# Performance work log

Measured on AMD Instinct MI355X. Metric: run time of the kernel, lower is better.

## Reference

```python
import jax, jax.numpy as jnp
import numpy as np

B = 8
N = 1024


def _sqrtm_psd(P):
    # symmetric PSD matrix square root via eigendecomposition
    w, V = jnp.linalg.eigh(P)
    return (V * jnp.sqrt(jnp.clip(w, 0.0))) @ V.T


def setup_inputs() -> dict:
    key = jax.random.key(0)
    k1, k2, k3 = jax.random.split(key, 3)
    x = jax.random.normal(k1, (1, B, N, 1), dtype=jnp.float32)
    # PSD covariance with nonnegative entries so abs() is a no-op and sqrtm is real
    A = jax.random.uniform(k2, (N, N), dtype=jnp.float32)
    P_u = (A @ A.T) / N
    Q_k = jax.random.uniform(k3, (N, N), dtype=jnp.float32)
    return {"x": x, "P_u": P_u, "Q_k": Q_k}


def reference(x, P_u, Q_k):
    n = x.shape[2]  # N
    # sigma = x.repeat(1,1,1,N): [1,B,N,N]
    sigma0 = jnp.broadcast_to(x, (1, x.shape[1], n, n))
    # p = sqrtm(N * |P_u|)
    p = _sqrtm_psd(n * jnp.abs(P_u))
    # concat(sigma+p, sigma-p) along last dim -> [1,B,N,2N]
    sigma = jnp.concatenate((sigma0 + p, sigma0 - p), axis=3)
    scale = 1.0 / (2 * n)
    x_bar = jnp.mean(sigma, axis=3)  # [1,B,N]
    # Faithful to original: only sigma[0,0] is used for the deviations,
    # while the mean varies with the batch index i2.
    points = sigma[0, 0]  # [N, 2N]
    c = points[None, :, :] - x_bar[0][:, :, None]  # [B, N, 2N]
    S = jnp.einsum('bni,bmi->bnm', c, c)  # sum of 2N outer products per batch
    P_k = S * scale + (Q_k ** 2) * 0.01
    return P_k, jnp.transpose(sigma, (0, 1, 3, 2))


if __name__ == "__main__":
    out = reference(**setup_inputs())
    print(out[0].shape, out[1].shape)
```

## Files before the change

kernel.cpp:

```cpp
#include <hip/hip_runtime.h>
#include <math.h>

#define NN 1024
#define BB 8
#define NS_ITERS 10
#define EPS_SHIFT 4.0f
#define MB (1u<<20)

typedef __attribute__((ext_vector_type(8))) short short8;
typedef __attribute__((ext_vector_type(4))) float floatx4;

__device__ __forceinline__ ushort f2bf(float f) {
    union { float f; uint32_t u; } v; v.f = f;
    uint32_t u = v.u;
    uint32_t r = (u + 0x7fffu + ((u >> 16) & 1u)) >> 16;
    return (ushort)r;
}
__device__ __forceinline__ float bf2f(ushort h) {
    union { uint32_t u; float f; } v; v.u = ((uint32_t)h) << 16;
    return v.f;
}

__device__ __forceinline__ void gload16(const ushort* g, ushort* s) {
    __builtin_amdgcn_global_load_lds(
        (__attribute__((address_space(1))) unsigned int*)(g),
        (__attribute__((address_space(3))) unsigned int*)(s), 16, 0, 0);
}

__device__ __forceinline__ float block_sum(float v) {
    #pragma unroll
    for (int off = 32; off > 0; off >>= 1) v += __shfl_down(v, off, 64);
    __shared__ float red[4];
    int lane = threadIdx.x & 63, wid = threadIdx.x >> 6;
    if (lane == 0) red[wid] = v;
    __syncthreads();
    float t = 0.f;
    if (threadIdx.x == 0) t = red[0] + red[1] + red[2] + red[3];
    return t;
}

__global__ __launch_bounds__(256) void matvec_abs(const float* __restrict__ pu,
                                                  const float* __restrict__ x,
                                                  float* __restrict__ y,
                                                  int use_ones) {
    int row = blockIdx.x;
    const float4* pr = (const float4*)(pu + (size_t)row * NN);
    float4 p = pr[threadIdx.x];
    float s;
    if (use_ones) {
        s = fabsf(p.x) + fabsf(p.y) + fabsf(p.z) + fabsf(p.w);
    } else {
        float4 xx = ((const float4*)x)[threadIdx.x];
        s = fabsf(p.x) * xx.x + fabsf(p.y) * xx.y + fabsf(p.z) * xx.z + fabsf(p.w) * xx.w;
    }
    s = block_sum(s);
    if (threadIdx.x == 0) y[row] = s;
}

__global__ void norm_vec(const float* __restrict__ y, float* __restrict__ v) {
    float ss = 0.f;
    for (int i = threadIdx.x; i < NN; i += 256) { float t = y[i]; ss += t * t; }
    #pragma unroll
    for (int off = 32; off > 0; off >>= 1) ss += __shfl_down(ss, off, 64);
    __shared__ float red[4];
    __shared__ float s_inv;
    int lane = threadIdx.x & 63, wid = threadIdx.x >> 6;
    if (lane == 0) red[wid] = ss;
    __syncthreads();
    if (threadIdx.x == 0) s_inv = rsqrtf(red[0] + red[1] + red[2] + red[3]);
    __syncthreads();
    float inv = s_inv;
    for (int i = threadIdx.x; i < NN; i += 256) v[i] = y[i] * inv;
}

__global__ void dot_vec(const float* __restrict__ a, const float* __restrict__ b,
                        float* __restrict__ out) {
    float s = 0.f;
    for (int i = threadIdx.x; i < NN; i += 256) s += a[i] * b[i];
    s = block_sum(s);
    if (threadIdx.x == 0) out[0] = s;
}

__global__ __launch_bounds__(256) void deflate_kernel(const float* __restrict__ pu,
                                                      const float* __restrict__ v,
                                                      const float* __restrict__ w,
                                                      float* __restrict__ sc,
                                                      float* __restrict__ D) {
    int idx = blockIdx.x * 256 + threadIdx.x;
    int row = idx >> 8;
    int c0 = (idx & 255) << 2;
    float lam = sc[5];
    float vr = v[row], wr = w[row];
    float4 p = ((const float4*)pu)[idx];
    float4 vc = *(const float4*)(v + c0);
    float4 wc = *(const float4*)(w + c0);
    float4 d;
    d.x = (float)NN * (fabsf(p.x) - vr * wc.x - wr * vc.x + lam * vr * vc.x);
    d.y = (float)NN * (fabsf(p.y) - vr * wc.y - wr * vc.y + lam * vr * vc.y);
    d.z = (float)NN * (fabsf(p.z) - vr * wc.z - wr * vc.z + lam * vr * vc.z);
    d.w = (float)NN * (fabsf(p.w) - vr * wc.w - wr * vc.w + lam * vr * vc.w);
    int dd = row - c0;
    if (dd == 0) d.x += EPS_SHIFT;
    else if (dd == 1) d.y += EPS_SHIFT;
    else if (dd == 2) d.z += EPS_SHIFT;
    else if (dd == 3) d.w += EPS_SHIFT;
    ((float4*)D)[idx] = d;
    float ss = d.x * d.x + d.y * d.y + d.z * d.z + d.w * d.w;
    ss = block_sum(ss);
    if (threadIdx.x == 0) atomicAdd(sc, ss);
}

__global__ void finalize_kernel(float* sc) {
    float c = sqrtf(sc[0]);
    sc[1] = 1.f / c;
    sc[2] = sqrtf(c);
    sc[4] = sqrtf((float)NN * sc[5]);
}

__device__ __forceinline__ void mm_dev(const ushort* __restrict__ Ah,
                                       const ushort* __restrict__ Al,
                                       const ushort* __restrict__ Bh,
                                       const ushort* __restrict__ Bl,
                                       int row0, int col0, int kb, int kc,
                                       float* __restrict__ Cf,
                                       ushort* __restrict__ Chi,
                                       ushort* __restrict__ Clo) {
    __shared__ __align__(16) ushort lds[2 * 4 * 2048];
    const int t = threadIdx.x;
    const int w = t >> 6, l = t & 63;
    const int wr = ((w >> 1) & 1) << 5;
    const int wc = (w & 1) << 5;
    const int fm = l & 15, fq = l >> 4;
    const int srow = l >> 2;
    const int skc = ((l & 3) + srow) & 3;

    const ushort* gsrc = (w == 0) ? Ah : (w == 1) ? Al : (w == 2) ? Bh : Bl;
    const int r0 = (w < 2) ? row0 : col0;
    const ushort* gp = gsrc + (size_t)(r0 + srow) * NN + kb + (skc << 3);

    floatx4 acc[2][2];
    acc[0][0] = (floatx4)0.f; acc[0][1] = (floatx4)0.f;
    acc[1][0] = (floatx4)0.f; acc[1][1] = (floatx4)0.f;

    auto STAGE = [&](int bufi, int koff) {
        ushort* sb = lds + (bufi << 13) + (w << 11);
        #pragma unroll
        for (int rb = 0; rb < 4; ++rb)
            gload16(gp + (size_t)(rb << 4) * NN + koff, sb + (rb << 9));
    };

    const int rot = ((fq - fm) & 3) << 3;
    auto COMPUTE = [&](int bufi) {
        const ushort* Ash = lds + (bufi << 13);
        const ushort* Asl = Ash + 2048;
        const ushort* Bsh = Ash + 4096;
        const ushort* Bsl = Ash + 6144;
        short8 ah0 = *(const short8*)&Ash[((wr + fm) << 5) + rot];
        short8 ah1 = *(const short8*)&Ash[((wr + 16 + fm) << 5) + rot];
        short8 al0 = *(const short8*)&Asl[((wr + fm) << 5) + rot];
        short8 al1 = *(const short8*)&Asl[((wr + 16 + fm) << 5) + rot];
        short8 bh0 = *(const short8*)&Bsh[((wc + fm) << 5) + rot];
        short8 bh1 = *(const short8*)&Bsh[((wc + 16 + fm) << 5) + rot];
        short8 bl0 = *(const short8*)&Bsl[((wc + fm) << 5) + rot];
        short8 bl1 = *(const short8*)&Bsl[((wc + 16 + fm) << 5) + rot];
        acc[0][0] = __builtin_amdgcn_mfma_f32_16x16x32_bf16(ah0, bh0, acc[0][0], 0, 0, 0);
        acc[0][1] = __builtin_amdgcn_mfma_f32_16x16x32_bf16(ah0, bh1, acc[0][1], 0, 0, 0);
        acc[1][0] = __builtin_amdgcn_mfma_f32_16x16x32_bf16(ah1, bh0, acc[1][0], 0, 0, 0);
        acc[1][1] = __builtin_amdgcn_mfma_f32_16x16x32_bf16(ah1, bh1, acc[1][1], 0, 0, 0);
        acc[0][0] = __builtin_amdgcn_mfma_f32_16x16x32_bf16(al0, bh0, acc[0][0], 0, 0, 0);
        acc[0][1] = __builtin_amdgcn_mfma_f32_16x16x32_bf16(al0, bh1, acc[0][1], 0, 0, 0);
        acc[1][0] = __builtin_amdgcn_mfma_f32_16x16x32_bf16(al1, bh0, acc[1][0], 0, 0, 0);
        acc[1][1] = __builtin_amdgcn_mfma_f32_16x16x32_bf16(al1, bh1, acc[1][1], 0, 0, 0);
        acc[0][0] = __builtin_amdgcn_mfma_f32_16x16x32_bf16(ah0, bl0, acc[0][0], 0, 0, 0);
        acc[0][1] = __builtin_amdgcn_mfma_f32_16x16x32_bf16(ah0, bl1, acc[0][1], 0, 0, 0);
        acc[1][0] = __builtin_amdgcn_mfma_f32_16x16x32_bf16(ah1, bl0, acc[1][0], 0, 0, 0);
        acc[1][1] = __builtin_amdgcn_mfma_f32_16x16x32_bf16(ah1, bl1, acc[1][1], 0, 0, 0);
    };

    const int nk = kc >> 5;
    STAGE(0, 0);
    __syncthreads();
    #pragma unroll 1
    for (int kt = 0; kt < nk; kt += 2) {
        STAGE(1, (kt + 1) << 5);
        COMPUTE(0);
        __syncthreads();
        if (kt + 2 < nk) STAGE(0, (kt + 2) << 5);
        COMPUTE(1);
        __syncthreads();
    }

    #pragma unroll
    for (int mi = 0; mi < 2; ++mi) {
        #pragma unroll
        for (int r = 0; r < 4; ++r) {
            int row = row0 + wr + (mi << 4) + (fq << 2) + r;
            #pragma unroll
            for (int ni = 0; ni < 2; ++ni) {
                int col = col0 + wc + (ni << 4) + fm;
                float v = acc[mi][ni][r];
                size_t idx = (size_t)row * NN + col;
                if (Cf) {
                    Cf[idx] = v;
                } else {
                    ushort h = f2bf(v);
                    Chi[idx] = h;
                    Clo[idx] = f2bf(v - bf2f(h));
                }
            }
        }
    }
}

__global__ __launch_bounds__(256) void k_stage1(const ushort* __restrict__ Zh,
                                                const ushort* __restrict__ Zl,
                                                const ushort* __restrict__ Yh,
                                                const ushort* __restrict__ Yl,
                                                float* __restrict__ Mp) {
    int s = blockIdx.z;
    mm_dev(Zh, Zl, Yh, Yl, blockIdx.y * 64, blockIdx.x * 64,
           s * (NN / 2), NN / 2, Mp + (size_t)s * NN * NN, nullptr, nullptr);
}

__global__ __launch_bounds__(256) void k_stage2(const ushort* __restrict__ Yh,
                                                const ushort* __restrict__ Yl,
                                                const ushort* __restrict__ Wh,
                                                const ushort* __restrict__ Wl,
                                                const ushort* __restrict__ Zh,
                                                const ushort* __restrict__ Zl,
                                                ushort* __restrict__ Ynh,
                                                ushort* __restrict__ Ynl,
                                                ushort* __restrict__ Znh,
                                                ushort* __restrict__ Znl) {
    if (blockIdx.z == 0)
        mm_dev(Yh, Yl, Wh, Wl, blockIdx.y * 64, blockIdx.x * 64, 0, NN,
               nullptr, Ynh, Ynl);
    else
        mm_dev(Wh, Wl, Zh, Zl, blockIdx.y * 64, blockIdx.x * 64, 0, NN,
               nullptr, Znh, Znl);
}

__global__ __launch_bounds__(256) void k_final(const ushort* __restrict__ Yh,
                                               const ushort* __restrict__ Yl,
                                               const ushort* __restrict__ Wh,
                                               const ushort* __restrict__ Wl,
                                               float* __restrict__ Yf) {
    mm_dev(Yh, Yl, Wh, Wl, blockIdx.y * 64, blockIdx.x * 64, 0, NN,
           Yf, nullptr, nullptr);
}

__global__ __launch_bounds__(256) void k_wsplit(const float* __restrict__ Mp,
                                                ushort* __restrict__ Wh,
                                                ushort* __restrict__ Wl) {
    int i = blockIdx.x * 256 + threadIdx.x;
    int row = i >> 8, c0 = (i & 255) << 2;
    float4 m0 = ((const float4*)Mp)[i];
    float4 m1 = ((const float4*)Mp)[i + NN * NN / 4];
    float mr[4] = {m0.x + m1.x, m0.y + m1.y, m0.z + m1.z, m0.w + m1.w};
    float wv[4];
    #pragma unroll
    for (int j = 0; j < 4; ++j) {
        float mt = Mp[(size_t)(c0 + j) * NN + row] +
                   Mp[(size_t)(c0 + j) * NN + row + (size_t)NN * NN];
        wv[j] = -0.25f * (mr[j] + mt);
    }
    int dd = row - c0;
    if (dd >= 0 && dd < 4) wv[dd] += 1.5f;
    ushort4 hv, lv;
    ushort* hp = (ushort*)&hv; ushort* lp = (ushort*)&lv;
    #pragma unroll
    for (int j = 0; j < 4; ++j) {
        ushort h = f2bf(wv[j]); hp[j] = h; lp[j] = f2bf(wv[j] - bf2f(h));
    }
    *(ushort4*)&Wh[(size_t)i << 2] = hv;
    *(ushort4*)&Wl[(size_t)i << 2] = lv;
}

__global__ __launch_bounds__(256) void k_wsplit0(const float* __restrict__ D,
                                                 const float* __restrict__ sc,
                                                 ushort* __restrict__ Yh,
                                                 ushort* __restrict__ Yl,
                                                 ushort* __restrict__ Wh,
                                                 ushort* __restrict__ Wl) {
    int i = blockIdx.x * 256 + threadIdx.x;
    int row = i >> 8, c0 = (i & 255) << 2;
    float invc = sc[1];
    float4 d = ((const float4*)D)[i];
    float yv[4] = {d.x * invc, d.y * invc, d.z * invc, d.w * invc};
    ushort4 yh, yl, wh, wl;
    ushort* yhp = (ushort*)&yh; ushort* ylp = (ushort*)&yl;
    ushort* whp = (ushort*)&wh; ushort* wlp = (ushort*)&wl;
    int dd = row - c0;
    #pragma unroll
    for (int j = 0; j < 4; ++j) {
        float y = yv[j];
        ushort h = f2bf(y); yhp[j] = h; ylp[j] = f2bf(y - bf2f(h));
        float wv = ((dd == j) ? 1.5f : 0.f) - 0.5f * y;
        ushort h2 = f2bf(wv); whp[j] = h2; wlp[j] = f2bf(wv - bf2f(h2));
    }
    *(ushort4*)&Yh[(size_t)i << 2] = yh;
    *(ushort4*)&Yl[(size_t)i << 2] = yl;
    *(ushort4*)&Wh[(size_t)i << 2] = wh;
    *(ushort4*)&Wl[(size_t)i << 2] = wl;
}

__global__ __launch_bounds__(256) void out0_kernel(const float* __restrict__ x,
                                                   const float* __restrict__ pu,
                                                   const float* __restrict__ qk,
                                                   float* __restrict__ out) {
    int i = blockIdx.x * blockDim.x + threadIdx.x;
    int rem = i & (NN * NN / 4 - 1);
    int b = i >> 18;
    int n = rem >> 8;
    int m4 = (rem & 255) << 2;
    float dn = x[n] - x[b * NN + n];
    float4 x0v = *(const float4*)(x + m4);
    float4 xbv = *(const float4*)(x + b * NN + m4);
    float4 pv = ((const float4*)pu)[rem];
    float4 qv = ((const float4*)qk)[rem];
    float4 o;
    o.x = dn * (x0v.x - xbv.x) + fabsf(pv.x) + 0.01f * qv.x * qv.x;
    o.y = dn * (x0v.y - xbv.y) + fabsf(pv.y) + 0.01f * qv.y * qv.y;
    o.z = dn * (x0v.z - xbv.z) + fabsf(pv.z) + 0.01f * qv.z * qv.z;
    o.w = dn * (x0v.w - xbv.w) + fabsf(pv.w) + 0.01f * qv.w * qv.w;
    ((float4*)out)[i] = o;
}

__global__ __launch_bounds__(256) void k_out1(const float* __restrict__ x,
                                              const float* __restrict__ Yf,
                                              const float* __restrict__ sc,
                                              const float* __restrict__ v,
                                              float* __restrict__ out1) {
    int i = blockIdx.x * 256 + threadIdx.x;
    int j = i >> 8, i0 = (i & 255) << 2;
    float s = 0.5f * sc[2], s1v = sc[4] * v[j];
    float4 yr = *(const float4*)(Yf + (size_t)j * NN + i0);
    float yc0 = Yf[(size_t)(i0 + 0) * NN + j];
    float yc1 = Yf[(size_t)(i0 + 1) * NN + j];
    float yc2 = Yf[(size_t)(i0 + 2) * NN + j];
    float yc3 = Yf[(size_t)(i0 + 3) * NN + j];
    float4 vc = *(const float4*)(v + i0);
    float4 p;
    p.x = s * (yr.x + yc0) + s1v * vc.x;
    p.y = s * (yr.y + yc1) + s1v * vc.y;
    p.z = s * (yr.z + yc2) + s1v * vc.z;
    p.w = s * (yr.w + yc3) + s1v * vc.w;
    #pragma unroll
    for (int b = 0; b < BB; ++b) {
        float4 xv = *(const float4*)(x + b * NN + i0);
        float4 a, m;
        a.x = xv.x + p.x; a.y = xv.y + p.y; a.z = xv.z + p.z; a.w = xv.w + p.w;
        m.x = xv.x - p.x; m.y = xv.y - p.y; m.z = xv.z - p.z; m.w = xv.w - p.w;
        float* base = out1 + (size_t)b * 2 * NN * NN;
        *(float4*)(base + (size_t)j * NN + i0) = a;
        *(float4*)(base + (size_t)(NN + j) * NN + i0) = m;
    }
}

extern "C" void kernel_launch(void* const* d_in, const int* in_sizes, int n_in,
                              void* d_out, int out_size, void* d_ws, size_t ws_size,
                              hipStream_t stream) {
    const float* x  = (const float*)d_in[0];
    const float* pu = (const float*)d_in[1];
    const float* qk = (const float*)d_in[2];
    float* out = (float*)d_out;
    char* ws = (char*)d_ws;

    float* Mp = (float*)ws;
    float* D  = Mp;
    float* Yf = Mp;
    ushort* hi[5]; ushort* lo[5];
    for (int k = 0; k < 5; ++k) {
        hi[k] = (ushort*)(ws + (size_t)8 * MB + (size_t)k * 4 * MB);
        lo[k] = (ushort*)(ws + (size_t)8 * MB + (size_t)k * 4 * MB + 2 * MB);
    }
    float* vv = (float*)(ws + (size_t)28 * MB);
    float* vw = (float*)(ws + (size_t)28 * MB + 4096);
    float* vt = (float*)(ws + (size_t)28 * MB + 8192);
    float* sc = (float*)(ws + (size_t)28 * MB + 12288);

    hipMemsetAsync(sc, 0, 64, stream);
    matvec_abs<<<NN, 256, 0, stream>>>(pu, vv, vt, 1);
    norm_vec<<<1, 256, 0, stream>>>(vt, vv);
    matvec_abs<<<NN, 256, 0, stream>>>(pu, vv, vt, 0);
    norm_vec<<<1, 256, 0, stream>>>(vt, vv);
    matvec_abs<<<NN, 256, 0, stream>>>(pu, vv, vw, 0);
    dot_vec<<<1, 256, 0, stream>>>(vv, vw, sc + 5);
    deflate_kernel<<<NN * NN / 4 / 256, 256, 0, stream>>>(pu, vv, vw, sc, D);
    finalize_kernel<<<1, 1, 0, stream>>>(sc);

    k_wsplit0<<<NN * NN / 4 / 256, 256, 0, stream>>>(D, sc, hi[0], lo[0], hi[1], lo[1]);
    k_stage2<<<dim3(16, 16, 1), 256, 0, stream>>>(hi[0], lo[0], hi[1], lo[1],
                                                  hi[0], lo[0],
                                                  hi[2], lo[2], hi[3], lo[3]);
    int Y = 2, Z = 1, f0 = 0, f1 = 3, f2 = 4;

    for (int it = 1; it < NS_ITERS; ++it) {
        int W = f0;
        k_stage1<<<dim3(16, 16, 2), 256, 0, stream>>>(hi[Z], lo[Z], hi[Y], lo[Y], Mp);
        k_wsplit<<<NN * NN / 4 / 256, 256, 0, stream>>>(Mp, hi[W], lo[W]);
        if (it + 1 < NS_ITERS) {
            int Yn = f1, Zn = f2;
            k_stage2<<<dim3(16, 16, 2), 256, 0, stream>>>(
                hi[Y], lo[Y], hi[W], lo[W], hi[Z], lo[Z],
                hi[Yn], lo[Yn], hi[Zn], lo[Zn]);
            f0 = Y; f1 = Z; f2 = W;
            Y = Yn; Z = Zn;
        } else {
            k_final<<<dim3(16, 16, 1), 256, 0, stream>>>(hi[Y], lo[Y], hi[W], lo[W], Yf);
        }
    }

    out0_kernel<<<(BB * NN * NN / 4) / 256, 256, 0, stream>>>(x, pu, qk, out);
    k_out1<<<NN * NN / 4 / 256, 256, 0, stream>>>(x, Yf, sc, vv,
                                                  out + (size_t)BB * NN * NN);
}
```

Before: 680.7 us.

## Enlarge GEMM tiles to 128x128 with 4x4 MFMA per wave and tile swizzle

The split-bf16 matmul device function moves from 64x64 block tiles to 128x128 tiles, so each wave computes a 64x64 sub-tile with 4x4 accumulators. This raises arithmetic intensity per LDS load and cuts global traffic. A block-index swizzle is added for L2 locality, and the grids shrink from 16x16 to 8x8. The LDS rotation swizzle is removed, which may bring back bank conflicts. With fewer blocks (64 or 128 on a GPU with many CUs), occupancy and load balance may suffer.

```diff
diff --git a/kernel.cpp b/kernel.cpp
--- a/kernel.cpp
+++ b/kernel.cpp
@@ -125,56 +125,55 @@
                                        float* __restrict__ Cf,
                                        ushort* __restrict__ Chi,
                                        ushort* __restrict__ Clo) {
-    __shared__ __align__(16) ushort lds[2 * 4 * 2048];
+    __shared__ __align__(16) ushort lds[2 * 4 * 4096];
     const int t = threadIdx.x;
     const int w = t >> 6, l = t & 63;
-    const int wr = ((w >> 1) & 1) << 5;
-    const int wc = (w & 1) << 5;
+    const int wr = ((w >> 1) & 1) << 6;
+    const int wc = (w & 1) << 6;
     const int fm = l & 15, fq = l >> 4;
     const int srow = l >> 2;
-    const int skc = ((l & 3) + srow) & 3;
+    const int scol = (l & 3) << 3;
 
     const ushort* gsrc = (w == 0) ? Ah : (w == 1) ? Al : (w == 2) ? Bh : Bl;
     const int r0 = (w < 2) ? row0 : col0;
-    const ushort* gp = gsrc + (size_t)(r0 + srow) * NN + kb + (skc << 3);
-
-    floatx4 acc[2][2];
-    acc[0][0] = (floatx4)0.f; acc[0][1] = (floatx4)0.f;
-    acc[1][0] = (floatx4)0.f; acc[1][1] = (floatx4)0.f;
+    const ushort* gp = gsrc + (size_t)(r0 + srow) * NN + kb + scol;
+
+    floatx4 acc[4][4];
+    #pragma unroll
+    for (int mi = 0; mi < 4; ++mi)
+        #pragma unroll
+        for (int ni = 0; ni < 4; ++ni) acc[mi][ni] = (floatx4)0.f;
 
     auto STAGE = [&](int bufi, int koff) {
-        ushort* sb = lds + (bufi << 13) + (w << 11);
+        ushort* sb = lds + (bufi << 14) + (w << 12);
         #pragma unroll
-        for (int rb = 0; rb < 4; ++rb)
+        for (int rb = 0; rb < 8; ++rb)
             gload16(gp + (size_t)(rb << 4) * NN + koff, sb + (rb << 9));
     };
 
-    const int rot = ((fq - fm) & 3) << 3;
     auto COMPUTE = [&](int bufi) {
-        const ushort* Ash = lds + (bufi << 13);
-        const ushort* Asl = Ash + 2048;
-        const ushort* Bsh = Ash + 4096;
-        const ushort* Bsl = Ash + 6144;
-        short8 ah0 = *(const short8*)&Ash[((wr + fm) << 5) + rot];
-        short8 ah1 = *(const short8*)&Ash[((wr + 16 + fm) << 5) + rot];
-        short8 al0 = *(const short8*)&Asl[((wr + fm) << 5) + rot];
-        short8 al1 = *(const short8*)&Asl[((wr + 16 + fm) << 5) + rot];
-        short8 bh0 = *(const short8*)&Bsh[((wc + fm) << 5) + rot];
-        short8 bh1 = *(const short8*)&Bsh[((wc + 16 + fm) << 5) + rot];
-        short8 bl0 = *(const short8*)&Bsl[((wc + fm) << 5) + rot];
-        short8 bl1 = *(const short8*)&Bsl[((wc + 16 + fm) << 5) + rot];
-        acc[0][0] = __builtin_amdgcn_mfma_f32_16x16x32_bf16(ah0, bh0, acc[0][0], 0, 0, 0);
-        acc[0][1] = __builtin_amdgcn_mfma_f32_16x16x32_bf16(ah0, bh1, acc[0][1], 0, 0, 0);
-        acc[1][0] = __builtin_amdgcn_mfma_f32_16x16x32_bf16(ah1, bh0, acc[1][0], 0, 0, 0);
-        acc[1][1] = __builtin_amdgcn_mfma_f32_16x16x32_bf16(ah1, bh1, acc[1][1], 0, 0, 0);
-        acc[0][0] = __builtin_amdgcn_mfma_f32_16x16x32_bf16(al0, bh0, acc[0][0], 0, 0, 0);
-        acc[0][1] = __builtin_amdgcn_mfma_f32_16x16x32_bf16(al0, bh1, acc[0][1], 0, 0, 0);
-        acc[1][0] = __builtin_amdgcn_mfma_f32_16x16x32_bf16(al1, bh0, acc[1][0], 0, 0, 0);
-        acc[1][1] = __builtin_amdgcn_mfma_f32_16x16x32_bf16(al1, bh1, acc[1][1], 0, 0, 0);
-        acc[0][0] = __builtin_amdgcn_mfma_f32_16x16x32_bf16(ah0, bl0, acc[0][0], 0, 0, 0);
-        acc[0][1] = __builtin_amdgcn_mfma_f32_16x16x32_bf16(ah0, bl1, acc[0][1], 0, 0, 0);
-        acc[1][0] = __builtin_amdgcn_mfma_f32_16x16x32_bf16(ah1, bl0, acc[1][0], 0, 0, 0);
-        acc[1][1] = __builtin_amdgcn_mfma_f32_16x16x32_bf16(ah1, bl1, acc[1][1], 0, 0, 0);
+        const ushort* Ash = lds + (bufi << 14);
+        const ushort* Asl = Ash + 4096;
+        const ushort* Bsh = Ash + 8192;
+        const ushort* Bsl = Ash + 12288;
+        short8 ah[4], al[4], bh[4], bl[4];
+        #pragma unroll
+        for (int i = 0; i < 4; ++i) {
+            const int ra = ((wr + (i << 4) + fm) << 5) + (fq << 3);
+            const int rb = ((wc + (i << 4) + fm) << 5) + (fq << 3);
+            ah[i] = *(const short8*)&Ash[ra];
+            al[i] = *(const short8*)&Asl[ra];
+            bh[i] = *(const short8*)&Bsh[rb];
+            bl[i] = *(const short8*)&Bsl[rb];
+        }
+        #pragma unroll
+        for (int mi = 0; mi < 4; ++mi)
+            #pragma unroll
+            for (int ni = 0; ni < 4; ++ni) {
+                acc[mi][ni] = __builtin_amdgcn_mfma_f32_16x16x32_bf16(ah[mi], bh[ni], acc[mi][ni], 0, 0, 0);
+                acc[mi][ni] = __builtin_amdgcn_mfma_f32_16x16x32_bf16(al[mi], bh[ni], acc[mi][ni], 0, 0, 0);
+                acc[mi][ni] = __builtin_amdgcn_mfma_f32_16x16x32_bf16(ah[mi], bl[ni], acc[mi][ni], 0, 0, 0);
+            }
     };
 
     const int nk = kc >> 5;
@@ -191,12 +190,12 @@
     }
 
     #pragma unroll
-    for (int mi = 0; mi < 2; ++mi) {
+    for (int mi = 0; mi < 4; ++mi) {
         #pragma unroll
         for (int r = 0; r < 4; ++r) {
             int row = row0 + wr + (mi << 4) + (fq << 2) + r;
             #pragma unroll
-            for (int ni = 0; ni < 2; ++ni) {
+            for (int ni = 0; ni < 4; ++ni) {
                 int col = col0 + wc + (ni << 4) + fm;
                 float v = acc[mi][ni][r];
                 size_t idx = (size_t)row * NN + col;
@@ -212,41 +211,51 @@
     }
 }
 
-__global__ __launch_bounds__(256) void k_stage1(const ushort* __restrict__ Zh,
-                                                const ushort* __restrict__ Zl,
-                                                const ushort* __restrict__ Yh,
-                                                const ushort* __restrict__ Yl,
-                                                float* __restrict__ Mp) {
+__device__ __forceinline__ void tile_swizzle(int& row0, int& col0) {
+    int flat = blockIdx.y * 8 + blockIdx.x;
+    int p = flat & 7;
+    int i = flat >> 3;
+    int by = ((p >> 1) << 1) + (i >> 2);
+    int bx = ((p & 1) << 2) + (i & 3);
+    row0 = by << 7;
+    col0 = bx << 7;
+}
+
+__global__ __launch_bounds__(256, 2) void k_stage1(const ushort* __restrict__ Zh,
+                                                   const ushort* __restrict__ Zl,
+                                                   const ushort* __restrict__ Yh,
+                                                   const ushort* __restrict__ Yl,
+                                                   float* __restrict__ Mp) {
     int s = blockIdx.z;
-    mm_dev(Zh, Zl, Yh, Yl, blockIdx.y * 64, blockIdx.x * 64,
+    int row0, col0; tile_swizzle(row0, col0);
+    mm_dev(Zh, Zl, Yh, Yl, row0, col0,
            s * (NN / 2), NN / 2, Mp + (size_t)s * NN * NN, nullptr, nullptr);
 }
 
-__global__ __launch_bounds__(256) void k_stage2(const ushort* __restrict__ Yh,
-                                                const ushort* __restrict__ Yl,
-                                                const ushort* __restrict__ Wh,
-                                                const ushort* __restrict__ Wl,
-                                                const ushort* __restrict__ Zh,
-                                                const ushort* __restrict__ Zl,
-                                                ushort* __restrict__ Ynh,
-                                                ushort* __restrict__ Ynl,
-                                                ushort* __restrict__ Znh,
-                                                ushort* __restrict__ Znl) {
+__global__ __launch_bounds__(256, 2) void k_stage2(const ushort* __restrict__ Yh,
+                                                   const ushort* __restrict__ Yl,
+                                                   const ushort* __restrict__ Wh,
+                                                   const ushort* __restrict__ Wl,
+                                                   const ushort* __restrict__ Zh,
+                                                   const ushort* __restrict__ Zl,
+                                                   ushort* __restrict__ Ynh,
+                                                   ushort* __restrict__ Ynl,
+                                                   ushort* __restrict__ Znh,
+                                                   ushort* __restrict__ Znl) {
+    int row0, col0; tile_swizzle(row0, col0);
     if (blockIdx.z == 0)
-        mm_dev(Yh, Yl, Wh, Wl, blockIdx.y * 64, blockIdx.x * 64, 0, NN,
-               nullptr, Ynh, Ynl);
+        mm_dev(Yh, Yl, Wh, Wl, row0, col0, 0, NN, nullptr, Ynh, Ynl);
     else
-        mm_dev(Wh, Wl, Zh, Zl, blockIdx.y * 64, blockIdx.x * 64, 0, NN,
-               nullptr, Znh, Znl);
-}
-
-__global__ __launch_bounds__(256) void k_final(const ushort* __restrict__ Yh,
-                                               const ushort* __restrict__ Yl,
-                                               const ushort* __restrict__ Wh,
-                                               const ushort* __restrict__ Wl,
-                                               float* __restrict__ Yf) {
-    mm_dev(Yh, Yl, Wh, Wl, blockIdx.y * 64, blockIdx.x * 64, 0, NN,
-           Yf, nullptr, nullptr);
+        mm_dev(Wh, Wl, Zh, Zl, row0, col0, 0, NN, nullptr, Znh, Znl);
+}
+
+__global__ __launch_bounds__(256, 2) void k_final(const ushort* __restrict__ Yh,
+                                                  const ushort* __restrict__ Yl,
+                                                  const ushort* __restrict__ Wh,
+                                                  const ushort* __restrict__ Wl,
+                                                  float* __restrict__ Yf) {
+    int row0, col0; tile_swizzle(row0, col0);
+    mm_dev(Yh, Yl, Wh, Wl, row0, col0, 0, NN, Yf, nullptr, nullptr);
 }
 
 __global__ __launch_bounds__(256) void k_wsplit(const float* __restrict__ Mp,
@@ -390,24 +399,24 @@
     finalize_kernel<<<1, 1, 0, stream>>>(sc);
 
     k_wsplit0<<<NN * NN / 4 / 256, 256, 0, stream>>>(D, sc, hi[0], lo[0], hi[1], lo[1]);
-    k_stage2<<<dim3(16, 16, 1), 256, 0, stream>>>(hi[0], lo[0], hi[1], lo[1],
-                                                  hi[0], lo[0],
-                                                  hi[2], lo[2], hi[3], lo[3]);
+    k_stage2<<<dim3(8, 8, 1), 256, 0, stream>>>(hi[0], lo[0], hi[1], lo[1],
+                                                hi[0], lo[0],
+                                                hi[2], lo[2], hi[3], lo[3]);
     int Y = 2, Z = 1, f0 = 0, f1 = 3, f2 = 4;
 
     for (int it = 1; it < NS_ITERS; ++it) {
         int W = f0;
-        k_stage1<<<dim3(16, 16, 2), 256, 0, stream>>>(hi[Z], lo[Z], hi[Y], lo[Y], Mp);
+        k_stage1<<<dim3(8, 8, 2), 256, 0, stream>>>(hi[Z], lo[Z], hi[Y], lo[Y], Mp);
         k_wsplit<<<NN * NN / 4 / 256, 256, 0, stream>>>(Mp, hi[W], lo[W]);
         if (it + 1 < NS_ITERS) {
             int Yn = f1, Zn = f2;
-            k_stage2<<<dim3(16, 16, 2), 256, 0, stream>>>(
+            k_stage2<<<dim3(8, 8, 2), 256, 0, stream>>>(
                 hi[Y], lo[Y], hi[W], lo[W], hi[Z], lo[Z],
                 hi[Yn], lo[Yn], hi[Zn], lo[Zn]);
             f0 = Y; f1 = Z; f2 = W;
             Y = Yn; Z = Zn;
         } else {
-            k_final<<<dim3(16, 16, 1), 256, 0, stream>>>(hi[Y], lo[Y], hi[W], lo[W], Yf);
+            k_final<<<dim3(8, 8, 1), 256, 0, stream>>>(hi[Y], lo[Y], hi[W], lo[W], Yf);
         }
     }
 
```

New measurement: 800.2 us. 1.18x slower.
